# Kernel optimization log

Measured on AMD Instinct MI355X. Metric: run time of the kernel, lower is better.

## Reference

```python
import jax, jax.numpy as jnp
import numpy as np

S_LEN = 1024; HIDDEN = 2048; VOCAB = 32000; DFF = 6144
NK = 8; NV = 16; DK = 128; DV = 128; CONV_K = 4
CONV_DIM = 2 * NK * DK + NV * DV  # 4096
NQ = 16; NKV = 2; HD = 128; MAX_KV = 4096; SP = 512; CHUNK = 64


def silu(x):
    return x * jax.nn.sigmoid(x)


def rmsnorm(x, w, eps=1e-6):
    xf = x.astype(jnp.float32)
    return (xf * jax.lax.rsqrt(jnp.mean(xf * xf, -1, keepdims=True) + eps)) * w


def gated_rmsnorm(x, z, w, eps=1e-6):
    xf = x.astype(jnp.float32) * silu(z.astype(jnp.float32))
    return (xf * jax.lax.rsqrt(jnp.mean(xf * xf, -1, keepdims=True) + eps)) * w


def rotate_half(x):
    a, b = jnp.split(x, 2, -1)
    return jnp.concatenate([-b, a], -1)


def chunk_gated_delta_rule(q, k, v, g, beta, init_state, chunk=CHUNK):
    # q,k: [B,S,H,Dk]; v: [B,S,H,Dv]; g,beta: [B,S,H]; init_state: [B,H,Dk,Dv]
    q = q / jnp.sqrt(jnp.sum(q * q, -1, keepdims=True) + 1e-6)  # qk l2norm
    k = k / jnp.sqrt(jnp.sum(k * k, -1, keepdims=True) + 1e-6)
    tr = lambda x: x.transpose(0, 2, 1, 3).astype(jnp.float32)
    q, k, v = tr(q), tr(k), tr(v)
    g = g.transpose(0, 2, 1).astype(jnp.float32)
    beta = beta.transpose(0, 2, 1).astype(jnp.float32)
    B, H, S, Dk = q.shape
    Dv = v.shape[-1]
    N = S // chunk  # S is a multiple of chunk here (no padding needed)
    q = q * Dk ** -0.5
    rc = lambda x: x.reshape(B, H, N, chunk, x.shape[-1])
    q, k, v = rc(q), rc(k), rc(v)
    g = jnp.cumsum(g.reshape(B, H, N, chunk), -1)  # cumulative log-decay within chunk
    beta = beta.reshape(B, H, N, chunk)
    kb = k * beta[..., None]
    vb = v * beta[..., None]
    ii = jnp.arange(chunk)
    lower = ii[:, None] >= ii[None, :]
    strict = ii[:, None] > ii[None, :]
    decay = jnp.where(lower, jnp.exp(g[..., :, None] - g[..., None, :]), 0.0)
    # strictly-lower A; T = (I - A)^{-1} (exact triangular solve == converged Neumann series)
    A = -jnp.where(strict, jnp.einsum('bhnik,bhnjk->bhnij', kb, k) * decay, 0.0)
    eye = jnp.eye(chunk, dtype=jnp.float32)
    T = jax.scipy.linalg.solve_triangular(eye - A, jnp.broadcast_to(eye, A.shape), lower=True)
    w = jnp.einsum('bhnij,bhnjd->bhnid', T, vb)
    kc = jnp.einsum('bhnij,bhnjd->bhnid', T, kb * jnp.exp(g)[..., None])
    mv = lambda x: jnp.moveaxis(x, 2, 0)

    def step(state, xs):
        qi, ki, wi, kci, gi, di = xs
        attn = jnp.where(lower, jnp.einsum('bhik,bhjk->bhij', qi, ki) * di, 0.0)
        v_new = wi - jnp.einsum('bhik,bhkd->bhid', kci, state)
        out = jnp.einsum('bhik,bhkd->bhid', qi * jnp.exp(gi)[..., None], state) \
            + jnp.einsum('bhij,bhjd->bhid', attn, v_new)
        gl = gi[..., -1]
        kd = ki * jnp.exp(gl[..., None] - gi)[..., None]
        state = state * jnp.exp(gl)[..., None, None] + jnp.einsum('bhik,bhid->bhkd', kd, v_new)
        return state, out

    final, outs = jax.lax.scan(step, init_state.astype(jnp.float32),
                               (mv(q), mv(k), mv(w), mv(kc), mv(g), mv(decay)))
    out = jnp.moveaxis(outs, 0, 2).reshape(B, H, S, Dv).transpose(0, 2, 1, 3)  # [B,S,H,Dv]
    return out, final


def mlp(x, gw, uw, dw):
    return (silu(x @ gw) * (x @ uw)) @ dw


def model_forward(input_ids, start_pos, rope_cos, rope_sin, attn_mask, conv_state, rec_state,
                  key_cache, value_cache, embed_w, dl_ln_w, dl_qkv_w, conv_w, conv_b, dl_z_w,
                  dl_b_w, dl_a_w, A_log, dt_bias, dn_norm_w, dl_out_w, dl_post_ln_w, dl_gate_w,
                  dl_up_w, dl_down_w, al_ln_w, q_w, q_norm_w, k_w, k_norm_w, v_w, o_w,
                  al_post_ln_w, al_gate_w, al_up_w, al_down_w, final_norm_w, lm_head_w):
    B, S = input_ids.shape
    hidden = embed_w[input_ids]
    # ---------------- DeltaNet (linear attention) layer ----------------
    res = hidden
    x = rmsnorm(hidden, dl_ln_w)
    mixed = (x @ dl_qkv_w).transpose(0, 2, 1)             # [B, CONV_DIM, S]
    padded = jnp.concatenate([conv_state, mixed], -1)      # [B, CONV_DIM, K+S]
    L = padded.shape[-1] - (CONV_K - 1)
    conv = conv_b[:, None] + sum(conv_w[:, kk][:, None] * padded[:, :, kk:kk + L]
                                 for kk in range(CONV_K))  # depthwise conv1d
    mixed = silu(conv[:, :, -S:]).transpose(0, 2, 1)
    new_conv = padded[:, :, -CONV_K:]
    kd = NK * DK
    qq = mixed[..., :kd].reshape(B, S, NK, DK)
    kk_ = mixed[..., kd:2 * kd].reshape(B, S, NK, DK)
    vv = mixed[..., 2 * kd:].reshape(B, S, NV, DV)
    z = (x @ dl_z_w).reshape(B, S, NV, DV)
    beta = jax.nn.sigmoid(x @ dl_b_w)
    a = (x @ dl_a_w).astype(jnp.float32)
    g = -jnp.exp(A_log.astype(jnp.float32)) * jax.nn.softplus(a + dt_bias)
    rep = NV // NK
    qq = jnp.repeat(qq, rep, axis=2)
    kk_ = jnp.repeat(kk_, rep, axis=2)
    core, new_rec = chunk_gated_delta_rule(qq, kk_, vv, g, beta, rec_state)
    core = gated_rmsnorm(core.reshape(-1, DV), z.reshape(-1, DV), dn_norm_w).reshape(B, S, NV * DV)
    hidden = res + core @ dl_out_w
    hidden = hidden + mlp(rmsnorm(hidden, dl_post_ln_w), dl_gate_w, dl_up_w, dl_down_w)
    # ---------------- Full attention layer (gated GQA, KV-cache scatter) ----------------
    res = hidden
    x = rmsnorm(hidden, al_ln_w)
    qg = (x @ q_w).reshape(B, S, NQ, 2 * HD)
    query, gate = jnp.split(qg, 2, -1)
    gate = gate.reshape(B, S, NQ * HD)
    query = rmsnorm(query, q_norm_w).transpose(0, 2, 1, 3)               # [B,NQ,S,HD]
    key_new = rmsnorm((x @ k_w).reshape(B, S, NKV, HD), k_norm_w).transpose(0, 2, 1, 3)
    value_new = (x @ v_w).reshape(B, S, NKV, HD).transpose(0, 2, 1, 3)
    c = rope_cos[:, None]
    sn = rope_sin[:, None]
    query = query * c + rotate_half(query) * sn
    key_new = key_new * c + rotate_half(key_new) * sn
    new_kc = jax.lax.dynamic_update_slice(key_cache, key_new, (0, 0, start_pos, 0))
    new_vc = jax.lax.dynamic_update_slice(value_cache, value_new, (0, 0, start_pos, 0))
    ng = NQ // NKV
    k_rep = jnp.repeat(new_kc, ng, axis=1)
    v_rep = jnp.repeat(new_vc, ng, axis=1)
    scores = jnp.einsum('bhsd,bhtd->bhst', query, k_rep) * HD ** -0.5 + attn_mask
    probs = jax.nn.softmax(scores.astype(jnp.float32), -1).astype(query.dtype)
    ao = jnp.einsum('bhst,bhtd->bhsd', probs, v_rep).transpose(0, 2, 1, 3).reshape(B, S, NQ * HD)
    ao = ao * jax.nn.sigmoid(gate)
    hidden = res + ao @ o_w
    hidden = hidden + mlp(rmsnorm(hidden, al_post_ln_w), al_gate_w, al_up_w, al_down_w)
    logits = rmsnorm(hidden, final_norm_w) @ lm_head_w
    return logits, new_conv, new_rec, new_kc, new_vc


def setup_inputs():
    key = jax.random.key(0)
    ks = iter(jax.random.split(key, 64))
    def rn(shape, s=0.02):
        return jax.random.normal(next(ks), shape, jnp.float32) * s
    input_ids = jax.random.randint(next(ks), (1, S_LEN), 0, VOCAB)
    inv = 1.0 / (10000.0 ** (jnp.arange(0, HD, 2, dtype=jnp.float32) / HD))
    pos = jnp.arange(SP, SP + S_LEN, dtype=jnp.float32)
    fr = pos[:, None] * inv[None, :]
    emb = jnp.concatenate([fr, fr], -1)
    rope_cos = jnp.cos(emb)[None]
    rope_sin = jnp.sin(emb)[None]
    qpos = SP + jnp.arange(S_LEN)
    kpos = jnp.arange(MAX_KV)
    attn_mask = jnp.where(kpos[None, :] <= qpos[:, None], 0.0, -1e9).astype(jnp.float32)[None, None]
    return dict(
        input_ids=input_ids, seq_len=S_LEN, start_pos=SP,
        rope_cos=rope_cos, rope_sin=rope_sin, attn_mask=attn_mask,
        conv_state=rn((1, CONV_DIM, CONV_K), 1.0), rec_state=rn((1, NV, DK, DV), 1.0),
        key_cache=rn((1, NKV, MAX_KV, HD), 1.0), value_cache=rn((1, NKV, MAX_KV, HD), 1.0),
        embed_w=rn((VOCAB, HIDDEN)), dl_ln_w=jnp.ones(HIDDEN),
        dl_qkv_w=rn((HIDDEN, CONV_DIM)), conv_w=rn((CONV_DIM, CONV_K), 0.3),
        conv_b=rn((CONV_DIM,)), dl_z_w=rn((HIDDEN, NV * DV)),
        dl_b_w=rn((HIDDEN, NV)), dl_a_w=rn((HIDDEN, NV)),
        A_log=jnp.log(jnp.linspace(1.0, 8.0, NV)), dt_bias=rn((NV,), 0.1),
        dn_norm_w=jnp.ones(DV), dl_out_w=rn((NV * DV, HIDDEN)),
        dl_post_ln_w=jnp.ones(HIDDEN), dl_gate_w=rn((HIDDEN, DFF)),
        dl_up_w=rn((HIDDEN, DFF)), dl_down_w=rn((DFF, HIDDEN)),
        al_ln_w=jnp.ones(HIDDEN), q_w=rn((HIDDEN, NQ * HD * 2)), q_norm_w=jnp.ones(HD),
        k_w=rn((HIDDEN, NKV * HD)), k_norm_w=jnp.ones(HD), v_w=rn((HIDDEN, NKV * HD)),
        o_w=rn((NQ * HD, HIDDEN)), al_post_ln_w=jnp.ones(HIDDEN),
        al_gate_w=rn((HIDDEN, DFF)), al_up_w=rn((HIDDEN, DFF)), al_down_w=rn((DFF, HIDDEN)),
        final_norm_w=jnp.ones(HIDDEN), lm_head_w=rn((HIDDEN, VOCAB)))


def reference(input_ids, seq_len, start_pos, rope_cos, rope_sin, attn_mask, conv_state,
              rec_state, key_cache, value_cache, embed_w, dl_ln_w, dl_qkv_w, conv_w, conv_b,
              dl_z_w, dl_b_w, dl_a_w, A_log, dt_bias, dn_norm_w, dl_out_w, dl_post_ln_w,
              dl_gate_w, dl_up_w, dl_down_w, al_ln_w, q_w, q_norm_w, k_w, k_norm_w, v_w, o_w,
              al_post_ln_w, al_gate_w, al_up_w, al_down_w, final_norm_w, lm_head_w):
    del seq_len  # unused in original forward body (padding bookkeeping only)
    return model_forward(input_ids, start_pos, rope_cos, rope_sin, attn_mask, conv_state,
                         rec_state, key_cache, value_cache, embed_w, dl_ln_w, dl_qkv_w, conv_w,
                         conv_b, dl_z_w, dl_b_w, dl_a_w, A_log, dt_bias, dn_norm_w, dl_out_w,
                         dl_post_ln_w, dl_gate_w, dl_up_w, dl_down_w, al_ln_w, q_w, q_norm_w,
                         k_w, k_norm_w, v_w, o_w, al_post_ln_w, al_gate_w, al_up_w, al_down_w,
                         final_norm_w, lm_head_w)
```

## Files before the change

kernel.cpp:

```cpp
#include <hip/hip_runtime.h>
#include <math.h>

#define S_LEN 1024
#define HIDN  2048
#define NVH   16
#define CDIM  4096
#define MAXKV 4096
#define SP    512

typedef __attribute__((ext_vector_type(4))) float f32x4v;
typedef _Float16 f16x8 __attribute__((ext_vector_type(8)));
typedef unsigned short ushort_t;

__device__ __forceinline__ unsigned int pack2h(float a, float b) {
  auto h = __builtin_amdgcn_cvt_pkrtz(a, b);
  return __builtin_bit_cast(unsigned int, h);
}
__device__ __forceinline__ ushort_t h16(float x) {
  auto v = __builtin_amdgcn_cvt_pkrtz(x, x);
  return (ushort_t)__builtin_bit_cast(unsigned int, v);
}
__device__ __forceinline__ void gload16(const void* g, void* l) {
  __builtin_amdgcn_global_load_lds(
      (const __attribute__((address_space(1))) void*)(g),
      (__attribute__((address_space(3))) void*)(l), 16, 0, 0);
}

template<int TM, bool ACC, bool FS>
__global__ __launch_bounds__(256) void gemm_f16(const float* __restrict__ A,
    const float* A2, const float* __restrict__ B,
    float* __restrict__ C, int M, int N, int K) {
  constexpr int MI = TM / 32;
  constexpr int AF = TM / 8;
  __shared__ unsigned int Al[4][TM][4];
  __shared__ unsigned int Bl[4][128][4];
  const int tid = threadIdx.x;
  const int gm = M / TM;
  const int nwg = gridDim.x;
  const int q = nwg >> 3, r = nwg & 7;
  const int xcd = blockIdx.x & 7, ii = blockIdx.x >> 3;
  const int lin = (xcd < r) ? (xcd * (q + 1) + ii)
                            : (r * (q + 1) + (xcd - r) * q + ii);
  const int m0 = (lin % gm) * TM;
  const int n0 = (lin / gm) * 128;
  const int wave = tid >> 6, lane = tid & 63;
  const int wm = (wave >> 1) * (TM / 2), wn = (wave & 1) * 64;
  const int lr = lane & 15, lg = lane >> 4;
  const int am  = (TM == 128) ? (tid >> 1) : (tid >> 2);
  const int akb = (TM == 128) ? ((tid & 1) * 2) : (tid & 3);
  const int bn = tid & 127, bkb = (tid >> 7) * 2;
  const float* Ap  = A + (size_t)(m0 + am) * K + akb * 8;
  const float* A2p = A2 + (size_t)(m0 + am) * K + akb * 8;
  const float* Bp = B + (size_t)(bkb * 8) * N + n0 + bn;
  float ar[AF], ar2[FS ? AF : 1], br[16];
  f32x4v acc[MI][4];
  #pragma unroll
  for (int i = 0; i < MI; ++i)
    #pragma unroll
    for (int j = 0; j < 4; ++j)
      #pragma unroll
      for (int r2 = 0; r2 < 4; ++r2) acc[i][j][r2] = 0.f;
  const int NT = K >> 5;
  #pragma unroll
  for (int q2 = 0; q2 < AF / 4; ++q2)
    *(float4*)&ar[q2 * 4] = *(const float4*)(Ap + q2 * 4);
  if (FS) {
    #pragma unroll
    for (int q2 = 0; q2 < AF / 4; ++q2)
      *(float4*)&ar2[q2 * 4] = *(const float4*)(A2p + q2 * 4);
  }
  #pragma unroll
  for (int j = 0; j < 16; ++j) br[j] = Bp[(size_t)j * N];
  for (int t = 0; t < NT; ++t) {
    __syncthreads();
    float av[AF];
    #pragma unroll
    for (int u = 0; u < AF; ++u) {
      float g = ar[u];
      av[u] = FS ? (g / (1.f + expf(-g))) * ar2[u] : g;
    }
    *(uint4*)&Al[akb][am][0] = make_uint4(
        pack2h(av[0], av[1]), pack2h(av[2], av[3]),
        pack2h(av[4], av[5]), pack2h(av[6], av[7]));
    if (TM == 128) {
      *(uint4*)&Al[akb + 1][am][0] = make_uint4(
          pack2h(av[8], av[9]), pack2h(av[10], av[11]),
          pack2h(av[12], av[13]), pack2h(av[14], av[15]));
    }
    *(uint4*)&Bl[bkb][bn][0] = make_uint4(
        pack2h(br[0], br[1]), pack2h(br[2], br[3]),
        pack2h(br[4], br[5]), pack2h(br[6], br[7]));
    *(uint4*)&Bl[bkb + 1][bn][0] = make_uint4(
        pack2h(br[8], br[9]), pack2h(br[10], br[11]),
        pack2h(br[12], br[13]), pack2h(br[14], br[15]));
    if (t + 1 < NT) {
      Ap += 32; A2p += 32; Bp += (size_t)32 * N;
      #pragma unroll
      for (int q2 = 0; q2 < AF / 4; ++q2)
        *(float4*)&ar[q2 * 4] = *(const float4*)(Ap + q2 * 4);
      if (FS) {
        #pragma unroll
        for (int q2 = 0; q2 < AF / 4; ++q2)
          *(float4*)&ar2[q2 * 4] = *(const float4*)(A2p + q2 * 4);
      }
      #pragma unroll
      for (int j = 0; j < 16; ++j) br[j] = Bp[(size_t)j * N];
    }
    __syncthreads();
    f16x8 af[MI], bfr[4];
    #pragma unroll
    for (int mi = 0; mi < MI; ++mi)
      af[mi] = *(const f16x8*)&Al[lg][wm + mi * 16 + lr][0];
    #pragma unroll
    for (int ni = 0; ni < 4; ++ni)
      bfr[ni] = *(const f16x8*)&Bl[lg][wn + ni * 16 + lr][0];
    #pragma unroll
    for (int mi = 0; mi < MI; ++mi)
      #pragma unroll
      for (int ni = 0; ni < 4; ++ni)
        acc[mi][ni] = __builtin_amdgcn_mfma_f32_16x16x32_f16(
            af[mi], bfr[ni], acc[mi][ni], 0, 0, 0);
  }
  #pragma unroll
  for (int mi = 0; mi < MI; ++mi) {
    #pragma unroll
    for (int ni = 0; ni < 4; ++ni) {
      const int rr = m0 + wm + mi * 16 + lg * 4;
      const int cc = n0 + wn + ni * 16 + lr;
      #pragma unroll
      for (int r2 = 0; r2 < 4; ++r2) {
        float* cp = C + (size_t)(rr + r2) * N + cc;
        if (ACC) *cp += acc[mi][ni][r2];
        else     *cp = acc[mi][ni][r2];
      }
    }
  }
}

__global__ __launch_bounds__(256) void embed_k(const int* __restrict__ ids,
    const float* __restrict__ emb, float* __restrict__ hid) {
  int t = blockIdx.x * 256 + threadIdx.x;
  int s = t >> 9;
  int c4 = (t & 511) * 4;
  *(float4*)(hid + (size_t)s * HIDN + c4) =
      *(const float4*)(emb + (size_t)ids[s] * HIDN + c4);
}

__global__ __launch_bounds__(256) void rmsnorm_k(const float* __restrict__ in,
    const float* __restrict__ w, float* __restrict__ out) {
  const int row = blockIdx.x;
  const float* ip = in + (size_t)row * HIDN;
  float ss = 0.f;
  for (int c = threadIdx.x * 4; c < HIDN; c += 1024) {
    float4 v = *(const float4*)(ip + c);
    ss += v.x * v.x + v.y * v.y + v.z * v.z + v.w * v.w;
  }
  #pragma unroll
  for (int o = 32; o > 0; o >>= 1) ss += __shfl_down(ss, o, 64);
  __shared__ float sred[4];
  if ((threadIdx.x & 63) == 0) sred[threadIdx.x >> 6] = ss;
  __syncthreads();
  float tot = sred[0] + sred[1] + sred[2] + sred[3];
  float sc = 1.f / sqrtf(tot * (1.f / HIDN) + 1e-6f);
  for (int c = threadIdx.x * 4; c < HIDN; c += 1024) {
    float4 v = *(const float4*)(ip + c);
    float4 o = make_float4(v.x * sc * w[c], v.y * sc * w[c + 1],
                           v.z * sc * w[c + 2], v.w * sc * w[c + 3]);
    *(float4*)(out + (size_t)row * HIDN + c) = o;
  }
}

__global__ __launch_bounds__(256) void newconv_k(const float* __restrict__ mixed,
                                                 float* __restrict__ nc) {
  int t = blockIdx.x * 256 + threadIdx.x;
  int c = t >> 2, kk = t & 3;
  nc[t] = mixed[(size_t)(1020 + kk) * CDIM + c];
}

__global__ __launch_bounds__(256) void conv_k(const float* __restrict__ mixed,
    const float* __restrict__ cstate, const float* __restrict__ cw,
    const float* __restrict__ cb, float* __restrict__ convo) {
  int idx = blockIdx.x * 256 + threadIdx.x;
  int c = idx & (CDIM - 1);
  int s = idx >> 12;
  float acc = cb[c];
  #pragma unroll
  for (int kk = 0; kk < 4; ++kk) {
    int j = s + 1 + kk;
    float pv = (j < 4) ? cstate[c * 4 + j] : mixed[(size_t)(j - 4) * CDIM + c];
    acc = fmaf(cw[c * 4 + kk], pv, acc);
  }
  convo[(size_t)s * CDIM + c] = acc / (1.f + expf(-acc));
}

__global__ __launch_bounds__(128) void qknorm_k(const float* __restrict__ convo,
    float* __restrict__ qn, float* __restrict__ kn) {
  const int b = blockIdx.x;
  const int h8 = b & 7, s = b >> 3;
  const int d = threadIdx.x;
  float qv = convo[(size_t)s * CDIM + h8 * 128 + d];
  float kv = convo[(size_t)s * CDIM + 1024 + h8 * 128 + d];
  __shared__ float sred[4];
  float pq = qv * qv, pk = kv * kv;
  #pragma unroll
  for (int o = 32; o > 0; o >>= 1) { pq += __shfl_down(pq, o, 64); pk += __shfl_down(pk, o, 64); }
  if ((d & 63) == 0) { sred[d >> 6] = pq; sred[2 + (d >> 6)] = pk; }
  __syncthreads();
  float sq = sred[0] + sred[1], sk = sred[2] + sred[3];
  qn[((size_t)h8 * S_LEN + s) * 128 + d] = qv * (1.f / sqrtf(sq + 1e-6f)) * 0.08838834764831845f;
  kn[((size_t)h8 * S_LEN + s) * 128 + d] = kv * (1.f / sqrtf(sk + 1e-6f));
}

__global__ __launch_bounds__(256) void betag_k(const float* __restrict__ x,
    const float* __restrict__ bw, const float* __restrict__ aw,
    const float* __restrict__ A_log, const float* __restrict__ dt_bias,
    float* __restrict__ beta, float* __restrict__ g) {
  __shared__ float sx[2048];
  __shared__ float rb[16][17], ra[16][17];
  const int s = blockIdx.x;
  for (int c = threadIdx.x; c < HIDN; c += 256) sx[c] = x[(size_t)s * HIDN + c];
  __syncthreads();
  const int h = threadIdx.x & 15, part = threadIdx.x >> 4;
  float accb = 0.f, acca = 0.f;
  for (int j = 0; j < 128; ++j) {
    int k = part * 128 + j;
    float xv = sx[k];
    accb = fmaf(xv, bw[(size_t)k * 16 + h], accb);
    acca = fmaf(xv, aw[(size_t)k * 16 + h], acca);
  }
  rb[part][h] = accb; ra[part][h] = acca;
  __syncthreads();
  if (threadIdx.x < 16) {
    const int hh = threadIdx.x;
    float sb = 0.f, sa = 0.f;
    for (int p = 0; p < 16; ++p) { sb += rb[p][hh]; sa += ra[p][hh]; }
    beta[(size_t)s * 16 + hh] = 1.f / (1.f + expf(-sb));
    float aa = sa + dt_bias[hh];
    float sp = (aa > 20.f) ? aa : log1pf(expf(aa));
    g[(size_t)s * 16 + hh] = -expf(A_log[hh]) * sp;
  }
}

__global__ __launch_bounds__(256) void delta_phase1(
    const float* __restrict__ qn, const float* __restrict__ kn,
    const float* __restrict__ convo, const float* __restrict__ beta,
    const float* __restrict__ g,
    float* __restrict__ Wb, ushort_t* __restrict__ KC16,
    ushort_t* __restrict__ Q16, ushort_t* __restrict__ K16,
    ushort_t* __restrict__ ATT16, float* __restrict__ GCb) {
  __shared__ float sK[64][129];
  __shared__ float sV[64][129];
  __shared__ float sQ[64][129];
  __shared__ float sT[64][64];
  __shared__ float sgc[64], sbeta[64], seg[64], sEgl[64];
  const int blk = blockIdx.x;
  const int n = blk & 15, h = blk >> 4;
  const int hq = h >> 1;
  const int r0 = n * 64;
  const int tid = threadIdx.x;
  const size_t hn = (size_t)h * 16 + n;
  for (int t = tid; t < 2048; t += 256) {
    int i = t >> 5, c4 = (t & 31) * 4;
    float4 kv = *(const float4*)(kn + ((size_t)hq * S_LEN + r0 + i) * 128 + c4);
    float4 qv = *(const float4*)(qn + ((size_t)hq * S_LEN + r0 + i) * 128 + c4);
    float4 vv = *(const float4*)(convo + (size_t)(r0 + i) * CDIM + 2048 + h * 128 + c4);
    sK[i][c4+0]=kv.x; sK[i][c4+1]=kv.y; sK[i][c4+2]=kv.z; sK[i][c4+3]=kv.w;
    sQ[i][c4+0]=qv.x; sQ[i][c4+1]=qv.y; sQ[i][c4+2]=qv.z; sQ[i][c4+3]=qv.w;
    sV[i][c4+0]=vv.x; sV[i][c4+1]=vv.y; sV[i][c4+2]=vv.z; sV[i][c4+3]=vv.w;
  }
  if (tid < 64) sbeta[tid] = beta[(size_t)(r0 + tid) * NVH + h];
  __syncthreads();
  if (tid == 0) {
    float acc = 0.f;
    for (int i = 0; i < 64; ++i) { acc += g[(size_t)(r0 + i) * NVH + h]; sgc[i] = acc; }
  }
  __syncthreads();
  if (tid < 64) {
    seg[tid] = expf(sgc[tid]);
    sEgl[tid] = expf(sgc[63] - sgc[tid]);
  }
  {
    const int ty = tid >> 4, tx = tid & 15;
    float a[4][4] = {};
    #pragma unroll 4
    for (int k = 0; k < 128; ++k) {
      float kr[4], kc_[4];
      #pragma unroll
      for (int di = 0; di < 4; ++di) kr[di] = sK[ty * 4 + di][k];
      #pragma unroll
      for (int dj = 0; dj < 4; ++dj) kc_[dj] = sK[tx * 4 + dj][k];
      #pragma unroll
      for (int di = 0; di < 4; ++di)
        #pragma unroll
        for (int dj = 0; dj < 4; ++dj)
          a[di][dj] = fmaf(kr[di], kc_[dj], a[di][dj]);
    }
    #pragma unroll
    for (int di = 0; di < 4; ++di) {
      int i = ty * 4 + di;
      #pragma unroll
      for (int dj = 0; dj < 4; ++dj) {
        int j = tx * 4 + dj;
        float v;
        if (i > j) v = sbeta[i] * a[di][dj] * expf(sgc[i] - sgc[j]);
        else v = (i == j) ? 1.f : 0.f;
        sT[i][j] = v;
      }
    }
  }
  __syncthreads();
  if (tid < 64) {
    const int c = tid;
    for (int i = 1; i < 64; ++i) {
      if (c <= i) {
        float acc = (c == i) ? 1.f : 0.f;
        for (int j = c; j < i; ++j) acc -= sT[i][j] * sT[j][c];
        sT[i][c] = acc;
      }
    }
  }
  __syncthreads();
  for (int t = tid; t < 1024; t += 256) {
    int i = t >> 4, dg = (t & 15) * 8;
    float aw[8] = {}, ak[8] = {};
    for (int j = 0; j <= i; ++j) {
      float tv = sT[i][j] * sbeta[j];
      float te = tv * seg[j];
      #pragma unroll
      for (int u = 0; u < 8; ++u) {
        aw[u] = fmaf(tv, sV[j][dg + u], aw[u]);
        ak[u] = fmaf(te, sK[j][dg + u], ak[u]);
      }
    }
    float* wp = Wb + (hn * 64 + i) * 128 + dg;
    *(float4*)wp = make_float4(aw[0], aw[1], aw[2], aw[3]);
    *(float4*)(wp + 4) = make_float4(aw[4], aw[5], aw[6], aw[7]);
    uint4 kc = make_uint4(pack2h(-ak[0], -ak[1]), pack2h(-ak[2], -ak[3]),
                          pack2h(-ak[4], -ak[5]), pack2h(-ak[6], -ak[7]));
    *(uint4*)(KC16 + hn * 8192 + (dg >> 3) * 512 + i * 8) = kc;
  }
  for (int t = tid; t < 1024; t += 256) {
    int i = t >> 4, dg = (t & 15) * 8;
    float e = seg[i];
    uint4 qv = make_uint4(
        pack2h(sQ[i][dg] * e, sQ[i][dg + 1] * e),
        pack2h(sQ[i][dg + 2] * e, sQ[i][dg + 3] * e),
        pack2h(sQ[i][dg + 4] * e, sQ[i][dg + 5] * e),
        pack2h(sQ[i][dg + 6] * e, sQ[i][dg + 7] * e));
    *(uint4*)(Q16 + hn * 8192 + (dg >> 3) * 512 + i * 8) = qv;
  }
  for (int t = tid; t < 1024; t += 256) {
    int kv = t & 127, ib = t >> 7;
    int i0 = ib * 8;
    uint4 kk2 = make_uint4(
        pack2h(sK[i0 + 0][kv] * sEgl[i0 + 0], sK[i0 + 1][kv] * sEgl[i0 + 1]),
        pack2h(sK[i0 + 2][kv] * sEgl[i0 + 2], sK[i0 + 3][kv] * sEgl[i0 + 3]),
        pack2h(sK[i0 + 4][kv] * sEgl[i0 + 4], sK[i0 + 5][kv] * sEgl[i0 + 5]),
        pack2h(sK[i0 + 6][kv] * sEgl[i0 + 6], sK[i0 + 7][kv] * sEgl[i0 + 7]));
    *(uint4*)(K16 + hn * 8192 + ib * 1024 + kv * 8) = kk2;
  }
  __syncthreads();
  {
    const int ty = tid >> 4, tx = tid & 15;
    float a[4][4] = {};
    #pragma unroll 4
    for (int k = 0; k < 128; ++k) {
      float qr[4], kc_[4];
      #pragma unroll
      for (int di = 0; di < 4; ++di) qr[di] = sQ[ty * 4 + di][k];
      #pragma unroll
      for (int dj = 0; dj < 4; ++dj) kc_[dj] = sK[tx * 4 + dj][k];
      #pragma unroll
      for (int di = 0; di < 4; ++di)
        #pragma unroll
        for (int dj = 0; dj < 4; ++dj)
          a[di][dj] = fmaf(qr[di], kc_[dj], a[di][dj]);
    }
    #pragma unroll
    for (int di = 0; di < 4; ++di) {
      int i = ty * 4 + di;
      #pragma unroll
      for (int dj = 0; dj < 4; ++dj) {
        int j = tx * 4 + dj;
        float v = 0.f;
        if (i >= j) v = a[di][dj] * expf(sgc[i] - sgc[j]);
        sT[i][j] = v;
      }
    }
  }
  __syncthreads();
  for (int t = tid; t < 512; t += 256) {
    int i = t >> 3, jb = t & 7;
    const float* ap = &sT[i][jb * 8];
    uint4 av = make_uint4(pack2h(ap[0], ap[1]), pack2h(ap[2], ap[3]),
                          pack2h(ap[4], ap[5]), pack2h(ap[6], ap[7]));
    *(uint4*)(ATT16 + hn * 4096 + jb * 512 + i * 8) = av;
  }
  if (tid < 64) GCb[hn * 64 + tid] = sgc[tid];
}

__global__ __launch_bounds__(256) void delta_phase2(
    const ushort_t* __restrict__ KC16, const ushort_t* __restrict__ Q16,
    const ushort_t* __restrict__ K16, const ushort_t* __restrict__ ATT16,
    const float* __restrict__ Wb, const float* __restrict__ GCb,
    const float* __restrict__ rec_state,
    float* __restrict__ core, float* __restrict__ new_rec) {
  __shared__ uint4 bufKC[1024];
  __shared__ uint4 bufQ[1024];
  __shared__ uint4 bufK[1024];
  __shared__ uint4 bufA[512];
  __shared__ uint4 bufS[512];
  __shared__ uint4 bufV[256];
  ushort_t* sKC = (ushort_t*)bufKC;
  ushort_t* sQ6 = (ushort_t*)bufQ;
  ushort_t* sK6 = (ushort_t*)bufK;
  ushort_t* sAT = (ushort_t*)bufA;
  ushort_t* sS  = (ushort_t*)bufS;
  ushort_t* sVn = (ushort_t*)bufV;
  const int h = blockIdx.x >> 2, ds = blockIdx.x & 3;
  const int d0 = ds * 32;
  const int tid = threadIdx.x;
  const int w = tid >> 6;
  const int lane = tid & 63, lr = lane & 15, lg = lane >> 4;
  const int rowS0 = w * 32;
  f32x4v aS[2][2];
  #pragma unroll
  for (int tm = 0; tm < 2; ++tm)
    #pragma unroll
    for (int tn = 0; tn < 2; ++tn)
      #pragma unroll
      for (int r = 0; r < 4; ++r) {
        int row = rowS0 + tm * 16 + lg * 4 + r;
        int col = tn * 16 + lr;
        aS[tm][tn][r] = rec_state[((size_t)h * 128 + row) * 128 + d0 + col];
      }
  for (int n = 0; n < 16; ++n) {
    const size_t hn = (size_t)h * 16 + n;
    const uint4* pKC = (const uint4*)(KC16 + hn * 8192);
    const uint4* pQ  = (const uint4*)(Q16  + hn * 8192);
    const uint4* pK  = (const uint4*)(K16  + hn * 8192);
    const uint4* pA  = (const uint4*)(ATT16 + hn * 4096);
    uint4 stKC[4], stQ[4], stK[4], stA[2];
    #pragma unroll
    for (int u = 0; u < 4; ++u) {
      stKC[u] = pKC[tid + u * 256];
      stQ[u]  = pQ[tid + u * 256];
      stK[u]  = pK[tid + u * 256];
    }
    #pragma unroll
    for (int u = 0; u < 2; ++u) stA[u] = pA[tid + u * 256];
    const float egl = expf(GCb[hn * 64 + 63]);
    float wseed[2][4];
    #pragma unroll
    for (int tn = 0; tn < 2; ++tn)
      #pragma unroll
      for (int r = 0; r < 4; ++r)
        wseed[tn][r] = Wb[(hn * 64 + (w * 16 + lg * 4 + r)) * 128 + d0 + tn * 16 + lr];
    #pragma unroll
    for (int tm = 0; tm < 2; ++tm)
      #pragma unroll
      for (int tn = 0; tn < 2; ++tn)
        #pragma unroll
        for (int r = 0; r < 4; ++r) {
          int row = rowS0 + tm * 16 + lg * 4 + r;
          int col = tn * 16 + lr;
          sS[(row >> 3) * 256 + col * 8 + (row & 7)] = h16(aS[tm][tn][r]);
        }
    #pragma unroll
    for (int u = 0; u < 4; ++u) {
      bufKC[tid + u * 256] = stKC[u];
      bufQ[tid + u * 256]  = stQ[u];
// ... 24 lines not shown
        int col = tn * 16 + lr;
        sVn[(row >> 3) * 256 + col * 8 + (row & 7)] = h16(aV[tn][r]);
      }
    __syncthreads();
    f32x4v aO[2];
    #pragma unroll
    for (int tn = 0; tn < 2; ++tn)
      #pragma unroll
      for (int r = 0; r < 4; ++r) aO[tn][r] = 0.f;
    #pragma unroll
    for (int c = 0; c < 4; ++c) {
      f16x8 a = *(const f16x8*)&sQ6[((c * 4 + lg) * 64 + w * 16 + lr) * 8];
      #pragma unroll
      for (int tn = 0; tn < 2; ++tn) {
        f16x8 b = *(const f16x8*)&sS[((c * 4 + lg) * 32 + tn * 16 + lr) * 8];
        aO[tn] = __builtin_amdgcn_mfma_f32_16x16x32_f16(a, b, aO[tn], 0, 0, 0);
      }
    }
    #pragma unroll
    for (int c = 0; c < 2; ++c) {
      f16x8 a = *(const f16x8*)&sAT[((c * 4 + lg) * 64 + w * 16 + lr) * 8];
      #pragma unroll
      for (int tn = 0; tn < 2; ++tn) {
        f16x8 b = *(const f16x8*)&sVn[((c * 4 + lg) * 32 + tn * 16 + lr) * 8];
        aO[tn] = __builtin_amdgcn_mfma_f32_16x16x32_f16(a, b, aO[tn], 0, 0, 0);
      }
    }
    #pragma unroll
    for (int tn = 0; tn < 2; ++tn)
      #pragma unroll
      for (int r = 0; r < 4; ++r) {
        int row = w * 16 + lg * 4 + r;
        core[(size_t)(n * 64 + row) * HIDN + h * 128 + d0 + tn * 16 + lr] = aO[tn][r];
      }
    #pragma unroll
    for (int tm = 0; tm < 2; ++tm)
      #pragma unroll
      for (int tn = 0; tn < 2; ++tn)
        #pragma unroll
        for (int r = 0; r < 4; ++r) aS[tm][tn][r] *= egl;
    #pragma unroll
    for (int tm = 0; tm < 2; ++tm) {
      #pragma unroll
      for (int c = 0; c < 2; ++c) {
        f16x8 a = *(const f16x8*)&sK6[((c * 4 + lg) * 128 + rowS0 + tm * 16 + lr) * 8];
        #pragma unroll
        for (int tn = 0; tn < 2; ++tn) {
          f16x8 b = *(const f16x8*)&sVn[((c * 4 + lg) * 32 + tn * 16 + lr) * 8];
          aS[tm][tn] = __builtin_amdgcn_mfma_f32_16x16x32_f16(a, b, aS[tm][tn], 0, 0, 0);
        }
      }
    }
    __syncthreads();
  }
  #pragma unroll
  for (int tm = 0; tm < 2; ++tm)
    #pragma unroll
    for (int tn = 0; tn < 2; ++tn)
      #pragma unroll
      for (int r = 0; r < 4; ++r) {
        int row = rowS0 + tm * 16 + lg * 4 + r;
        int col = tn * 16 + lr;
        new_rec[((size_t)h * 128 + row) * 128 + d0 + col] = aS[tm][tn][r];
      }
}

__global__ __launch_bounds__(128) void gatedrms_k(float* __restrict__ core,
    const float* __restrict__ z, const float* __restrict__ w) {
  const int b = blockIdx.x;
  const int h = b & 15, s = b >> 4;
  const int d = threadIdx.x;
  size_t idx = (size_t)s * HIDN + h * 128 + d;
  float cv = core[idx], zv = z[idx];
  float xf = cv * (zv / (1.f + expf(-zv)));
  __shared__ float sred[2];
  float ps = xf * xf;
  #pragma unroll
  for (int o = 32; o > 0; o >>= 1) ps += __shfl_down(ps, o, 64);
  if ((d & 63) == 0) sred[d >> 6] = ps;
  __syncthreads();
  float ss = sred[0] + sred[1];
  core[idx] = xf * (1.f / sqrtf(ss * (1.f / 128.f) + 1e-6f)) * w[d];
}

__global__ __launch_bounds__(128) void qrope_k(const float* __restrict__ qg,
    const float* __restrict__ qnw, const float* __restrict__ cosb,
    const float* __restrict__ sinb, float* __restrict__ qhat,
    float* __restrict__ agate) {
  const int b = blockIdx.x;
  const int h = b & 15, s = b >> 4;
  const int d = threadIdx.x;
  float qv = qg[(size_t)s * 4096 + h * 256 + d];
  float gv = qg[(size_t)s * 4096 + h * 256 + 128 + d];
  __shared__ float sred[2];
  float ps = qv * qv;
  #pragma unroll
  for (int o = 32; o > 0; o >>= 1) ps += __shfl_down(ps, o, 64);
  if ((d & 63) == 0) sred[d >> 6] = ps;
  __syncthreads();
  float ss = sred[0] + sred[1];
  float qn_ = qv * (1.f / sqrtf(ss * (1.f / 128.f) + 1e-6f)) * qnw[d];
  __shared__ float tmp[128];
  tmp[d] = qn_;
  __syncthreads();
  float other = tmp[d ^ 64];
  float rh = (d < 64) ? -other : other;
  float c = cosb[(size_t)s * 128 + d];
  float sn = sinb[(size_t)s * 128 + d];
  qhat[((size_t)h * S_LEN + s) * 128 + d] = qn_ * c + rh * sn;
  agate[(size_t)s * HIDN + h * 128 + d] = gv;
}

__global__ __launch_bounds__(128) void kvrope_k(const float* __restrict__ kraw,
    const float* __restrict__ vraw, const float* __restrict__ knw,
    const float* __restrict__ cosb, const float* __restrict__ sinb,
    float* __restrict__ kcache, float* __restrict__ vcache) {
  const int b = blockIdx.x;
  const int h2 = b & 1, s = b >> 1;
  const int d = threadIdx.x;
  float kv = kraw[(size_t)s * 256 + h2 * 128 + d];
  __shared__ float sred[2];
  float ps = kv * kv;
  #pragma unroll
  for (int o = 32; o > 0; o >>= 1) ps += __shfl_down(ps, o, 64);
  if ((d & 63) == 0) sred[d >> 6] = ps;
  __syncthreads();
  float ss = sred[0] + sred[1];
  float kn_ = kv * (1.f / sqrtf(ss * (1.f / 128.f) + 1e-6f)) * knw[d];
  __shared__ float tmp[128];
  tmp[d] = kn_;
  __syncthreads();
  float other = tmp[d ^ 64];
  float rh = (d < 64) ? -other : other;
  size_t row = (size_t)h2 * MAXKV + SP + s;
  kcache[row * 128 + d] = kn_ * cosb[(size_t)s * 128 + d] + rh * sinb[(size_t)s * 128 + d];
  vcache[row * 128 + d] = vraw[(size_t)s * 256 + h2 * 128 + d];
}

__global__ __launch_bounds__(256) void kv16_k(const float* __restrict__ kc,
    const float* __restrict__ vc, ushort_t* __restrict__ KV16) {
  const int b = blockIdx.x;
  const int kt = b % 24, h2 = b / 24;
  const int tid = threadIdx.x;
  const float* Kb = kc + ((size_t)h2 * MAXKV + kt * 64) * 128;
  const float* Vb = vc + ((size_t)h2 * MAXKV + kt * 64) * 128;
  ushort_t* Ko = KV16 + ((size_t)h2 * 24 + kt) * 8192;
  ushort_t* Vo = KV16 + 393216 + ((size_t)h2 * 24 + kt) * 8192;
  #pragma unroll
  for (int it = 0; it < 4; ++it) {
    int tt = tid + it * 256;
    int row = tt >> 4, kb = tt & 15;
    float4 a = *(const float4*)(Kb + row * 128 + kb * 8);
    float4 c = *(const float4*)(Kb + row * 128 + kb * 8 + 4);
    *(uint4*)(Ko + ((size_t)kb * 64 + row) * 8) = make_uint4(
        pack2h(a.x, a.y), pack2h(a.z, a.w), pack2h(c.x, c.y), pack2h(c.z, c.w));
  }
  #pragma unroll
  for (int it = 0; it < 4; ++it) {
    int tt = tid + it * 256;
    int key = tt >> 4, dg = tt & 15;
    float4 a = *(const float4*)(Vb + key * 128 + dg * 8);
    float4 c = *(const float4*)(Vb + key * 128 + dg * 8 + 4);
    int base = (key >> 3) * 1024 + (key & 7);
    Vo[base + (dg * 8 + 0) * 8] = h16(a.x);
    Vo[base + (dg * 8 + 1) * 8] = h16(a.y);
    Vo[base + (dg * 8 + 2) * 8] = h16(a.z);
    Vo[base + (dg * 8 + 3) * 8] = h16(a.w);
    Vo[base + (dg * 8 + 4) * 8] = h16(c.x);
    Vo[base + (dg * 8 + 5) * 8] = h16(c.y);
    Vo[base + (dg * 8 + 6) * 8] = h16(c.z);
    Vo[base + (dg * 8 + 7) * 8] = h16(c.w);
  }
}

__global__ __launch_bounds__(256) void attn_k(const float* __restrict__ qhat,
    const ushort_t* __restrict__ KV16,
    const float* __restrict__ agate, float* __restrict__ ao) {
  __shared__ unsigned int Ql[16][64][4];
  __shared__ unsigned int Kl[16][64][4];
  __shared__ unsigned int Vl[8][128][4];
  __shared__ unsigned int Pl[8][64][4];
  const int h = blockIdx.x >> 4, qb = blockIdx.x & 15;
  const int hkv = h >> 3;
  const int tid = threadIdx.x;
  const int wave = tid >> 6, lane = tid & 63;
  const int lr = lane & 15, lg = lane >> 4;
  const float SCALE = 0.08838834764831845f;
  const float* Qb = qhat + ((size_t)h * S_LEN + qb * 64) * 128;
  #pragma unroll
  for (int it = 0; it < 4; ++it) {
    int tt = tid + it * 256;
    int row = tt >> 4, kb = tt & 15;
    float4 a = *(const float4*)(Qb + row * 128 + kb * 8);
    float4 b = *(const float4*)(Qb + row * 128 + kb * 8 + 4);
    *(uint4*)&Ql[kb][row][0] = make_uint4(
        pack2h(a.x * SCALE, a.y * SCALE), pack2h(a.z * SCALE, a.w * SCALE),
        pack2h(b.x * SCALE, b.y * SCALE), pack2h(b.z * SCALE, b.w * SCALE));
  }
  float m_run[4], l_run[4];
  #pragma unroll
  for (int r = 0; r < 4; ++r) { m_run[r] = -3.0e38f; l_run[r] = 0.f; }
  f32x4v accO[8];
  #pragma unroll
  for (int nd = 0; nd < 8; ++nd)
    #pragma unroll
    for (int r = 0; r < 4; ++r) accO[nd][r] = 0.f;
  const int ntiles = 9 + qb;
  for (int kt = 0; kt < ntiles; ++kt) {
    __syncthreads();
    const ushort_t* Ks = KV16 + ((size_t)hkv * 24 + kt) * 8192;
    const ushort_t* Vs = KV16 + 393216 + ((size_t)hkv * 24 + kt) * 8192;
    #pragma unroll
    for (int i2 = 0; i2 < 4; ++i2) {
      int c = wave * 4 + i2;
      gload16(Ks + (size_t)c * 512 + lane * 8, (char*)Kl + c * 1024);
      gload16(Vs + (size_t)c * 512 + lane * 8, (char*)Vl + c * 1024);
    }
    __syncthreads();
    f32x4v accS[4];
    #pragma unroll
    for (int ni = 0; ni < 4; ++ni)
      #pragma unroll
      for (int r = 0; r < 4; ++r) accS[ni][r] = 0.f;
    #pragma unroll
    for (int c = 0; c < 4; ++c) {
      f16x8 aq = *(const f16x8*)&Ql[c * 4 + lg][wave * 16 + lr][0];
      #pragma unroll
      for (int ni = 0; ni < 4; ++ni) {
        f16x8 bk = *(const f16x8*)&Kl[c * 4 + lg][ni * 16 + lr][0];
        accS[ni] = __builtin_amdgcn_mfma_f32_16x16x32_f16(aq, bk, accS[ni], 0, 0, 0);
      }
    }
    const bool boundary = (kt == ntiles - 1);
    float alpha[4];
    #pragma unroll
    for (int r = 0; r < 4; ++r) {
      const int qrow = wave * 16 + lg * 4 + r;
      float tm = -3.0e38f;
      #pragma unroll
      for (int ni = 0; ni < 4; ++ni) {
        if (boundary && (ni * 16 + lr) > qrow) accS[ni][r] = -3.0e38f;
        tm = fmaxf(tm, accS[ni][r]);
      }
      tm = fmaxf(tm, __shfl_xor(tm, 1, 64));
      tm = fmaxf(tm, __shfl_xor(tm, 2, 64));
      tm = fmaxf(tm, __shfl_xor(tm, 4, 64));
      tm = fmaxf(tm, __shfl_xor(tm, 8, 64));
      float mnew = fmaxf(m_run[r], tm);
      alpha[r] = expf(m_run[r] - mnew);
      m_run[r] = mnew;
      float ls = 0.f;
      #pragma unroll
      for (int ni = 0; ni < 4; ++ni) {
        float p = expf(accS[ni][r] - mnew);
        accS[ni][r] = p;
        ls += p;
      }
      ls += __shfl_xor(ls, 1, 64);
      ls += __shfl_xor(ls, 2, 64);
      ls += __shfl_xor(ls, 4, 64);
      ls += __shfl_xor(ls, 8, 64);
      l_run[r] = l_run[r] * alpha[r] + ls;
    }
    {
      _Float16* pp = (_Float16*)Pl;
      #pragma unroll
      for (int ni = 0; ni < 4; ++ni) {
        int key = ni * 16 + lr;
        int base = (key >> 3) * 512 + (key & 7);
        #pragma unroll
        for (int r = 0; r < 4; ++r) {
          int q = wave * 16 + lg * 4 + r;
          pp[base + q * 8] = (_Float16)accS[ni][r];
        }
      }
    }
    #pragma unroll
    for (int nd = 0; nd < 8; ++nd)
      #pragma unroll
      for (int r = 0; r < 4; ++r) accO[nd][r] *= alpha[r];
    #pragma unroll
    for (int c2 = 0; c2 < 2; ++c2) {
      f16x8 ap = *(const f16x8*)&Pl[c2 * 4 + lg][wave * 16 + lr][0];
      #pragma unroll
      for (int nd = 0; nd < 8; ++nd) {
        f16x8 bv = *(const f16x8*)&Vl[c2 * 4 + lg][nd * 16 + lr][0];
        accO[nd] = __builtin_amdgcn_mfma_f32_16x16x32_f16(ap, bv, accO[nd], 0, 0, 0);
      }
    }
  }
  #pragma unroll
  for (int r = 0; r < 4; ++r) {
    const int s = qb * 64 + wave * 16 + lg * 4 + r;
    const float inv = 1.f / l_run[r];
    #pragma unroll
    for (int nd = 0; nd < 8; ++nd) {
      int d = nd * 16 + lr;
      float gv = agate[(size_t)s * HIDN + h * 128 + d];
      ao[(size_t)s * HIDN + h * 128 + d] = accO[nd][r] * inv * (1.f / (1.f + expf(-gv)));
    }
  }
}

static inline void gemm128(const float* A, const float* B, float* C,
                           int M, int N, int K, bool acc, hipStream_t st) {
  dim3 g((N / 128) * (M / 128));
  if (acc) hipLaunchKernelGGL((gemm_f16<128, true,  false>), g, dim3(256), 0, st, A, A, B, C, M, N, K);
  else     hipLaunchKernelGGL((gemm_f16<128, false, false>), g, dim3(256), 0, st, A, A, B, C, M, N, K);
}
static inline void gemm64(const float* A, const float* B, float* C,
                          int M, int N, int K, bool acc, hipStream_t st) {
  dim3 g((N / 128) * (M / 64));
  if (acc) hipLaunchKernelGGL((gemm_f16<64, true,  false>), g, dim3(256), 0, st, A, A, B, C, M, N, K);
  else     hipLaunchKernelGGL((gemm_f16<64, false, false>), g, dim3(256), 0, st, A, A, B, C, M, N, K);
}
static inline void gemm_dn(const float* G, const float* U, const float* B, float* C,
                           int M, int N, int K, hipStream_t st) {
  dim3 g((N / 128) * (M / 64));
  hipLaunchKernelGGL((gemm_f16<64, true, true>), g, dim3(256), 0, st, G, U, B, C, M, N, K);
}

extern "C" void kernel_launch(void* const* d_in, const int* in_sizes, int n_in,
                              void* d_out, int out_size, void* d_ws, size_t ws_size,
                              hipStream_t stream) {
  (void)in_sizes; (void)n_in; (void)out_size; (void)ws_size;
  const int*   ids         = (const int*)  d_in[0];
  const float* rope_cos    = (const float*)d_in[3];
  const float* rope_sin    = (const float*)d_in[4];
  const float* conv_state  = (const float*)d_in[6];
  const float* rec_state   = (const float*)d_in[7];
  const float* key_cache   = (const float*)d_in[8];
  const float* value_cache = (const float*)d_in[9];
  const float* embed_w     = (const float*)d_in[10];
  const float* dl_ln_w     = (const float*)d_in[11];
  const float* dl_qkv_w    = (const float*)d_in[12];
  const float* conv_w      = (const float*)d_in[13];
  const float* conv_b      = (const float*)d_in[14];
  const float* dl_z_w      = (const float*)d_in[15];
  const float* dl_b_w      = (const float*)d_in[16];
  const float* dl_a_w      = (const float*)d_in[17];
  const float* A_log       = (const float*)d_in[18];
  const float* dt_bias     = (const float*)d_in[19];
  const float* dn_norm_w   = (const float*)d_in[20];
  const float* dl_out_w    = (const float*)d_in[21];
  const float* dl_post_ln  = (const float*)d_in[22];
  const float* dl_gate_w   = (const float*)d_in[23];
  const float* dl_up_w     = (const float*)d_in[24];
  const float* dl_down_w   = (const float*)d_in[25];
  const float* al_ln_w     = (const float*)d_in[26];
  const float* q_w         = (const float*)d_in[27];
  const float* q_norm_w    = (const float*)d_in[28];
  const float* k_w         = (const float*)d_in[29];
  const float* k_norm_w    = (const float*)d_in[30];
  const float* v_w         = (const float*)d_in[31];
  const float* o_w         = (const float*)d_in[32];
  const float* al_post_ln  = (const float*)d_in[33];
  const float* al_gate_w   = (const float*)d_in[34];
  const float* al_up_w     = (const float*)d_in[35];
  const float* al_down_w   = (const float*)d_in[36];
  const float* final_norm  = (const float*)d_in[37];
  const float* lm_head_w   = (const float*)d_in[38];

  float* out = (float*)d_out;
  float* logits   = out;
  float* new_conv = out + 32768000;
  float* new_rec  = out + 32784384;
  float* new_kc   = out + 33046528;
  float* new_vc   = out + 34095104;

  float* A_mixed = logits;
  float* A_convo = logits + 4194304;
  float* A_z     = logits + 8388608;
  float* A_qn    = logits + 10485760;
  float* A_kn    = logits + 11534336;
  float* A_w     = logits + 12582912;
  float* A_kc    = logits + 14680064;
  float* A_att   = logits + 16777216;
  float* A_gc    = logits + 17825792;
  float* A_core  = logits + 17842176;
  float* A_big0  = logits + 19939328;
  float* A_big1  = logits + 26230784;
  float* A_qhat  = A_big1;
  float* A_gate  = A_big1 + 2097152;
  float* A_ao    = A_big1 + 4194304;
  float* A_kraw  = A_mixed;
  float* A_vraw  = A_mixed + 262144;

  ushort_t* KC16  = (ushort_t*)A_kc;
  ushort_t* K16   = (ushort_t*)A_kc + 2097152;
  ushort_t* Q16   = (ushort_t*)A_att;
  ushort_t* ATT16 = (ushort_t*)A_big0;
  ushort_t* KV16  = (ushort_t*)(A_big0 + 4194304);

  float* ws     = (float*)d_ws;
  float* W_hid  = ws;
  float* W_x    = ws + 2097152;
  float* W_beta = ws + 4194304;
  float* W_g    = ws + 4210688;

  hipLaunchKernelGGL(embed_k, dim3(2048), dim3(256), 0, stream, ids, embed_w, W_hid);
  hipLaunchKernelGGL(rmsnorm_k, dim3(1024), dim3(256), 0, stream, W_hid, dl_ln_w, W_x);
  gemm128(W_x, dl_qkv_w, A_mixed, 1024, 4096, 2048, false, stream);
  hipLaunchKernelGGL(newconv_k, dim3(64), dim3(256), 0, stream, A_mixed, new_conv);
  hipLaunchKernelGGL(conv_k, dim3(16384), dim3(256), 0, stream,
                     A_mixed, conv_state, conv_w, conv_b, A_convo);
  gemm64(W_x, dl_z_w, A_z, 1024, 2048, 2048, false, stream);
  hipLaunchKernelGGL(betag_k, dim3(1024), dim3(256), 0, stream,
                     W_x, dl_b_w, dl_a_w, A_log, dt_bias, W_beta, W_g);
  hipLaunchKernelGGL(qknorm_k, dim3(8192), dim3(128), 0, stream, A_convo, A_qn, A_kn);
  hipLaunchKernelGGL(delta_phase1, dim3(256), dim3(256), 0, stream,
                     A_qn, A_kn, A_convo, W_beta, W_g,
                     A_w, KC16, Q16, K16, ATT16, A_gc);
  hipLaunchKernelGGL(delta_phase2, dim3(64), dim3(256), 0, stream,
                     KC16, Q16, K16, ATT16, A_w, A_gc, rec_state, A_core, new_rec);
  hipLaunchKernelGGL(gatedrms_k, dim3(16384), dim3(128), 0, stream, A_core, A_z, dn_norm_w);
  gemm64(A_core, dl_out_w, W_hid, 1024, 2048, 2048, true, stream);
  hipLaunchKernelGGL(rmsnorm_k, dim3(1024), dim3(256), 0, stream, W_hid, dl_post_ln, W_x);
  gemm64(W_x, dl_gate_w, A_big0, 1024, 6144, 2048, false, stream);
  gemm64(W_x, dl_up_w,   A_big1, 1024, 6144, 2048, false, stream);
  gemm_dn(A_big0, A_big1, dl_down_w, W_hid, 1024, 2048, 6144, stream);
  hipLaunchKernelGGL(rmsnorm_k, dim3(1024), dim3(256), 0, stream, W_hid, al_ln_w, W_x);
  gemm128(W_x, q_w, A_big0, 1024, 4096, 2048, false, stream);
  hipLaunchKernelGGL(qrope_k, dim3(16384), dim3(128), 0, stream,
                     A_big0, q_norm_w, rope_cos, rope_sin, A_qhat, A_gate);
  gemm64(W_x, k_w, A_kraw, 1024, 256, 2048, false, stream);
  gemm64(W_x, v_w, A_vraw, 1024, 256, 2048, false, stream);
  hipMemcpyAsync(new_kc, key_cache,   (size_t)2 * MAXKV * 128 * 4, hipMemcpyDeviceToDevice, stream);
  hipMemcpyAsync(new_vc, value_cache, (size_t)2 * MAXKV * 128 * 4, hipMemcpyDeviceToDevice, stream);
  hipLaunchKernelGGL(kvrope_k, dim3(2048), dim3(128), 0, stream,
                     A_kraw, A_vraw, k_norm_w, rope_cos, rope_sin, new_kc, new_vc);
  hipLaunchKernelGGL(kv16_k, dim3(48), dim3(256), 0, stream, new_kc, new_vc, KV16);
  hipLaunchKernelGGL(attn_k, dim3(256), dim3(256), 0, stream,
                     A_qhat, KV16, A_gate, A_ao);
  gemm64(A_ao, o_w, W_hid, 1024, 2048, 2048, true, stream);
  hipLaunchKernelGGL(rmsnorm_k, dim3(1024), dim3(256), 0, stream, W_hid, al_post_ln, W_x);
  gemm64(W_x, al_gate_w, A_big0, 1024, 6144, 2048, false, stream);
  gemm64(W_x, al_up_w,   A_big1, 1024, 6144, 2048, false, stream);
  gemm_dn(A_big0, A_big1, al_down_w, W_hid, 1024, 2048, 6144, stream);
  hipLaunchKernelGGL(rmsnorm_k, dim3(1024), dim3(256), 0, stream, W_hid, final_norm, W_x);
  gemm128(W_x, lm_head_w, logits, 1024, 32000, 2048, false, stream);
}
```

Measured before the change: 1.667 ms.

## Emit pre-packed fp16 activation panels from rmsnorm and add GEMM consuming them

rmsnorm now also writes its output as fp16 in a panel-tiled layout, 64-row panels with 32-wide k tiles. A new gemm_h kernel loads A tiles straight into LDS with global_load_lds and skips the per-tile fp32-to-fp16 conversion. All GEMMs that take a normalized input (qkv, z, gate/up, q, k, v, lm_head) switch to it, which cuts A-side read bandwidth and conversion work. Its risks are a workspace-size fallback path, overwriting A_qn when the workspace is small, and an lm_head fallback to the old kernel.

```diff
diff --git a/kernel.cpp b/kernel.cpp
--- a/kernel.cpp
+++ b/kernel.cpp
@@ -24,6 +24,92 @@
   __builtin_amdgcn_global_load_lds(
       (const __attribute__((address_space(1))) void*)(g),
       (__attribute__((address_space(3))) void*)(l), 16, 0, 0);
+}
+
+template<int TM>
+__global__ __launch_bounds__(256) void gemm_h(const ushort_t* __restrict__ A16,
+    const float* __restrict__ B, float* __restrict__ C, int M, int N, int K) {
+  constexpr int MI = TM / 32;
+  __shared__ ushort_t Al[TM * 32];
+  __shared__ unsigned int Bl[4][128][4];
+  const int tid = threadIdx.x;
+  const int gm = M / TM;
+  const int nwg = gridDim.x;
+  const int q = nwg >> 3, r = nwg & 7;
+  const int xcd = blockIdx.x & 7, ii = blockIdx.x >> 3;
+  const int lin = (xcd < r) ? (xcd * (q + 1) + ii)
+                            : (r * (q + 1) + (xcd - r) * q + ii);
+  const int m0 = (lin % gm) * TM;
+  const int n0 = (lin / gm) * 128;
+  const int wave = tid >> 6, lane = tid & 63;
+  const int wm = (wave >> 1) * (TM / 2), wn = (wave & 1) * 64;
+  const int lr = lane & 15, lg = lane >> 4;
+  const int bn = tid & 127, bkb = (tid >> 7) * 2;
+  const size_t panstride = (size_t)(K >> 5) * 2048;
+  const ushort_t* Apan = A16 + (size_t)(m0 >> 6) * panstride;
+  const float* Bp = B + (size_t)(bkb * 8) * N + n0 + bn;
+  float br[16];
+  f32x4v acc[MI][4];
+  #pragma unroll
+  for (int i = 0; i < MI; ++i)
+    #pragma unroll
+    for (int j = 0; j < 4; ++j)
+      #pragma unroll
+      for (int r2 = 0; r2 < 4; ++r2) acc[i][j][r2] = 0.f;
+  const int NT = K >> 5;
+  #pragma unroll
+  for (int j = 0; j < 16; ++j) br[j] = Bp[(size_t)j * N];
+  for (int t = 0; t < NT; ++t) {
+    __syncthreads();
+    if (TM == 128) {
+      #pragma unroll
+      for (int i2 = 0; i2 < 2; ++i2) {
+        int c = wave * 2 + i2;
+        int kb = c >> 1, half = c & 1;
+        gload16(Apan + half * panstride + (size_t)t * 2048 + kb * 512 + lane * 8,
+                Al + kb * 1024 + half * 512);
+      }
+    } else {
+      int kb = wave;
+      gload16(Apan + (size_t)t * 2048 + kb * 512 + lane * 8, Al + kb * 512);
+    }
+    *(uint4*)&Bl[bkb][bn][0] = make_uint4(
+        pack2h(br[0], br[1]), pack2h(br[2], br[3]),
+        pack2h(br[4], br[5]), pack2h(br[6], br[7]));
+    *(uint4*)&Bl[bkb + 1][bn][0] = make_uint4(
+        pack2h(br[8], br[9]), pack2h(br[10], br[11]),
+        pack2h(br[12], br[13]), pack2h(br[14], br[15]));
+    if (t + 1 < NT) {
+      Bp += (size_t)32 * N;
+      #pragma unroll
+      for (int j = 0; j < 16; ++j) br[j] = Bp[(size_t)j * N];
+    }
+    __syncthreads();
+    f16x8 af[MI], bfr[4];
+    #pragma unroll
+    for (int mi = 0; mi < MI; ++mi)
+      af[mi] = *(const f16x8*)&Al[lg * (TM * 8) + (wm + mi * 16 + lr) * 8];
+    #pragma unroll
+    for (int ni = 0; ni < 4; ++ni)
+      bfr[ni] = *(const f16x8*)&Bl[lg][wn + ni * 16 + lr][0];
+    #pragma unroll
+    for (int mi = 0; mi < MI; ++mi)
+      #pragma unroll
+      for (int ni = 0; ni < 4; ++ni)
+        acc[mi][ni] = __builtin_amdgcn_mfma_f32_16x16x32_f16(
+            af[mi], bfr[ni], acc[mi][ni], 0, 0, 0);
+  }
+  #pragma unroll
+  for (int mi = 0; mi < MI; ++mi) {
+    #pragma unroll
+    for (int ni = 0; ni < 4; ++ni) {
+      const int rr = m0 + wm + mi * 16 + lg * 4;
+      const int cc = n0 + wn + ni * 16 + lr;
+      #pragma unroll
+      for (int r2 = 0; r2 < 4; ++r2)
+        C[(size_t)(rr + r2) * N + cc] = acc[mi][ni][r2];
+    }
+  }
 }
 
 template<int TM, bool ACC, bool FS>
@@ -147,7 +233,8 @@
 }
 
 __global__ __launch_bounds__(256) void rmsnorm_k(const float* __restrict__ in,
-    const float* __restrict__ w, float* __restrict__ out) {
+    const float* __restrict__ w, float* __restrict__ out,
+    ushort_t* __restrict__ x16) {
   const int row = blockIdx.x;
   const float* ip = in + (size_t)row * HIDN;
   float ss = 0.f;
@@ -162,11 +249,16 @@
   __syncthreads();
   float tot = sred[0] + sred[1] + sred[2] + sred[3];
   float sc = 1.f / sqrtf(tot * (1.f / HIDN) + 1e-6f);
+  const int m = row & 63, mp = row >> 6;
+  ushort_t* xb = x16 + (size_t)mp * (HIDN >> 5) * 2048 + m * 8;
   for (int c = threadIdx.x * 4; c < HIDN; c += 1024) {
     float4 v = *(const float4*)(ip + c);
     float4 o = make_float4(v.x * sc * w[c], v.y * sc * w[c + 1],
                            v.z * sc * w[c + 2], v.w * sc * w[c + 3]);
     *(float4*)(out + (size_t)row * HIDN + c) = o;
+    int kt = c >> 5, kb = (c >> 3) & 3, j = c & 7;
+    *(uint2*)(xb + (size_t)kt * 2048 + kb * 512 + j) =
+        make_uint2(pack2h(o.x, o.y), pack2h(o.z, o.w));
   }
 }
 
@@ -797,6 +889,16 @@
   }
 }
 
+static inline void gemmh128(const ushort_t* A16, const float* B, float* C,
+                            int M, int N, int K, hipStream_t st) {
+  dim3 g((N / 128) * (M / 128));
+  hipLaunchKernelGGL((gemm_h<128>), g, dim3(256), 0, st, A16, B, C, M, N, K);
+}
+static inline void gemmh64(const ushort_t* A16, const float* B, float* C,
+                           int M, int N, int K, hipStream_t st) {
+  dim3 g((N / 128) * (M / 64));
+  hipLaunchKernelGGL((gemm_h<64>), g, dim3(256), 0, st, A16, B, C, M, N, K);
+}
 static inline void gemm128(const float* A, const float* B, float* C,
                            int M, int N, int K, bool acc, hipStream_t st) {
   dim3 g((N / 128) * (M / 128));
@@ -818,7 +920,7 @@
 extern "C" void kernel_launch(void* const* d_in, const int* in_sizes, int n_in,
                               void* d_out, int out_size, void* d_ws, size_t ws_size,
                               hipStream_t stream) {
-  (void)in_sizes; (void)n_in; (void)out_size; (void)ws_size;
+  (void)in_sizes; (void)n_in; (void)out_size;
   const int*   ids         = (const int*)  d_in[0];
   const float* rope_cos    = (const float*)d_in[3];
   const float* rope_sin    = (const float*)d_in[4];
@@ -893,13 +995,17 @@
   float* W_beta = ws + 4194304;
   float* W_g    = ws + 4210688;
 
+  const bool ws_ok = (ws_size >= (size_t)21102592 + 65536);
+  ushort_t* X16 = ws_ok ? (ushort_t*)(ws + 4227072)
+                        : (ushort_t*)A_qn;
+
   hipLaunchKernelGGL(embed_k, dim3(2048), dim3(256), 0, stream, ids, embed_w, W_hid);
-  hipLaunchKernelGGL(rmsnorm_k, dim3(1024), dim3(256), 0, stream, W_hid, dl_ln_w, W_x);
-  gemm128(W_x, dl_qkv_w, A_mixed, 1024, 4096, 2048, false, stream);
+  hipLaunchKernelGGL(rmsnorm_k, dim3(1024), dim3(256), 0, stream, W_hid, dl_ln_w, W_x, X16);
+  gemmh128(X16, dl_qkv_w, A_mixed, 1024, 4096, 2048, stream);
   hipLaunchKernelGGL(newconv_k, dim3(64), dim3(256), 0, stream, A_mixed, new_conv);
   hipLaunchKernelGGL(conv_k, dim3(16384), dim3(256), 0, stream,
                      A_mixed, conv_state, conv_w, conv_b, A_convo);
-  gemm64(W_x, dl_z_w, A_z, 1024, 2048, 2048, false, stream);
+  gemmh64(X16, dl_z_w, A_z, 1024, 2048, 2048, stream);
   hipLaunchKernelGGL(betag_k, dim3(1024), dim3(256), 0, stream,
                      W_x, dl_b_w, dl_a_w, A_log, dt_bias, W_beta, W_g);
   hipLaunchKernelGGL(qknorm_k, dim3(8192), dim3(128), 0, stream, A_convo, A_qn, A_kn);
@@ -910,16 +1016,16 @@
                      KC16, Q16, K16, ATT16, A_w, A_gc, rec_state, A_core, new_rec);
   hipLaunchKernelGGL(gatedrms_k, dim3(16384), dim3(128), 0, stream, A_core, A_z, dn_norm_w);
   gemm64(A_core, dl_out_w, W_hid, 1024, 2048, 2048, true, stream);
-  hipLaunchKernelGGL(rmsnorm_k, dim3(1024), dim3(256), 0, stream, W_hid, dl_post_ln, W_x);
-  gemm64(W_x, dl_gate_w, A_big0, 1024, 6144, 2048, false, stream);
-  gemm64(W_x, dl_up_w,   A_big1, 1024, 6144, 2048, false, stream);
+  hipLaunchKernelGGL(rmsnorm_k, dim3(1024), dim3(256), 0, stream, W_hid, dl_post_ln, W_x, X16);
+  gemmh64(X16, dl_gate_w, A_big0, 1024, 6144, 2048, stream);
+  gemmh64(X16, dl_up_w,   A_big1, 1024, 6144, 2048, stream);
   gemm_dn(A_big0, A_big1, dl_down_w, W_hid, 1024, 2048, 6144, stream);
-  hipLaunchKernelGGL(rmsnorm_k, dim3(1024), dim3(256), 0, stream, W_hid, al_ln_w, W_x);
-  gemm128(W_x, q_w, A_big0, 1024, 4096, 2048, false, stream);
+  hipLaunchKernelGGL(rmsnorm_k, dim3(1024), dim3(256), 0, stream, W_hid, al_ln_w, W_x, X16);
+  gemmh128(X16, q_w, A_big0, 1024, 4096, 2048, stream);
   hipLaunchKernelGGL(qrope_k, dim3(16384), dim3(128), 0, stream,
                      A_big0, q_norm_w, rope_cos, rope_sin, A_qhat, A_gate);
-  gemm64(W_x, k_w, A_kraw, 1024, 256, 2048, false, stream);
-  gemm64(W_x, v_w, A_vraw, 1024, 256, 2048, false, stream);
+  gemmh64(X16, k_w, A_kraw, 1024, 256, 2048, stream);
+  gemmh64(X16, v_w, A_vraw, 1024, 256, 2048, stream);
   hipMemcpyAsync(new_kc, key_cache,   (size_t)2 * MAXKV * 128 * 4, hipMemcpyDeviceToDevice, stream);
   hipMemcpyAsync(new_vc, value_cache, (size_t)2 * MAXKV * 128 * 4, hipMemcpyDeviceToDevice, stream);
   hipLaunchKernelGGL(kvrope_k, dim3(2048), dim3(128), 0, stream,
@@ -928,10 +1034,11 @@
   hipLaunchKernelGGL(attn_k, dim3(256), dim3(256), 0, stream,
                      A_qhat, KV16, A_gate, A_ao);
   gemm64(A_ao, o_w, W_hid, 1024, 2048, 2048, true, stream);
-  hipLaunchKernelGGL(rmsnorm_k, dim3(1024), dim3(256), 0, stream, W_hid, al_post_ln, W_x);
-  gemm64(W_x, al_gate_w, A_big0, 1024, 6144, 2048, false, stream);
-  gemm64(W_x, al_up_w,   A_big1, 1024, 6144, 2048, false, stream);
+  hipLaunchKernelGGL(rmsnorm_k, dim3(1024), dim3(256), 0, stream, W_hid, al_post_ln, W_x, X16);
+  gemmh64(X16, al_gate_w, A_big0, 1024, 6144, 2048, stream);
+  gemmh64(X16, al_up_w,   A_big1, 1024, 6144, 2048, stream);
   gemm_dn(A_big0, A_big1, al_down_w, W_hid, 1024, 2048, 6144, stream);
-  hipLaunchKernelGGL(rmsnorm_k, dim3(1024), dim3(256), 0, stream, W_hid, final_norm, W_x);
-  gemm128(W_x, lm_head_w, logits, 1024, 32000, 2048, false, stream);
-}
+  hipLaunchKernelGGL(rmsnorm_k, dim3(1024), dim3(256), 0, stream, W_hid, final_norm, W_x, X16);
+  if (ws_ok) gemmh128(X16, lm_head_w, logits, 1024, 32000, 2048, stream);
+  else       gemm128(W_x, lm_head_w, logits, 1024, 32000, 2048, false, stream);
+}
```

Measured after the change: 1.663 ms. About the same (-0.2%).
